# Performance work log

Hardware: AMD Instinct MI355X
Metric: run time of the kernel (lower is better)

The kernel has to match this reference:

```python
import jax, jax.numpy as jnp
import numpy as np

NUM_HEADS = 16
HEAD_DIM = 64  # embedding_dim 1024 / 16


def setup_inputs() -> dict:
    key = jax.random.key(0)
    k1, k2, k3, k4 = jax.random.split(key, 4)
    B, S, D = 2, 2048, 1024
    return {
        "query": jax.random.normal(k1, (B, S, D), dtype=jnp.float32),
        "key": jax.random.normal(k2, (B, S, D), dtype=jnp.float32),
        "value": jax.random.normal(k3, (B, S, D), dtype=jnp.float32),
        "W_out": jax.random.normal(k4, (D, D), dtype=jnp.float32) * (1.0 / np.sqrt(D)),
        "b_out": jnp.zeros((D,), dtype=jnp.float32),
    }


def reference(query, key, value, W_out, b_out):
    B, S, D = query.shape
    H, hd = NUM_HEADS, HEAD_DIM
    # NOTE: original forward never applies q_fc/k_fc/v_fc (transform ignores fc)
    q = query.reshape(B, S, H, hd).transpose(0, 2, 1, 3)  # [B,H,S,hd]
    k = key.reshape(B, S, H, hd).transpose(0, 2, 1, 3)
    v = value.reshape(B, S, H, hd).transpose(0, 2, 1, 3)
    scores = jnp.einsum("bhqd,bhkd->bhqk", q, k) / jnp.sqrt(jnp.float32(hd))
    probs = jax.nn.softmax(scores, axis=-1)  # mask=None, dropout=None
    ctx = jnp.einsum("bhqk,bhkd->bhqd", probs, v)
    ctx = ctx.transpose(0, 2, 1, 3).reshape(B, S, D)
    return ctx @ W_out.T + b_out
```

## Files before the change

### kernel.cpp

```cpp
#include <hip/hip_runtime.h>
#include <stdint.h>

#define NB 2
#define SEQ 2048
#define DIM 1024
#define NH 16
#define HD 64

typedef __attribute__((ext_vector_type(4))) float f32x4;
typedef __attribute__((ext_vector_type(16))) float f32x16;
typedef __attribute__((ext_vector_type(8))) short s16x8;
typedef __attribute__((ext_vector_type(4))) short s16x4;
typedef __attribute__((ext_vector_type(8))) __bf16 bf16x8;

static __device__ __forceinline__ short f2bf_rne(float x) {
  uint32_t u = __float_as_uint(x);
  u += 0x7fffu + ((u >> 16) & 1u);
  return (short)(u >> 16);
}
static __device__ __forceinline__ float bfbits2f(short h) {
  return __uint_as_float(((uint32_t)(uint16_t)h) << 16);
}
static __device__ __forceinline__ bf16x8 ldfrag(const short* p) {
  bf16x8 r;
  __builtin_memcpy(&r, p, 16);
  return r;
}
static __device__ __forceinline__ void glds16(const short* g, short* l) {
  __builtin_amdgcn_global_load_lds(
      (const __attribute__((address_space(1))) uint32_t*)g,
      (__attribute__((address_space(3))) uint32_t*)l, 16, 0, 0);
}

__global__ __launch_bounds__(256) void prep_kv(const float* __restrict__ K,
                                               const float* __restrict__ V,
                                               short* __restrict__ Kh,
                                               short* __restrict__ Vt) {
  __shared__ float vtile[64][65];
  const int tid = threadIdx.x;
  const int t0 = blockIdx.x * 64;
  const int bh = blockIdx.y;
  const int b = bh >> 4, h = bh & 15;

#pragma unroll
  for (int i = 0; i < 4; ++i) {
    int f = tid + 256 * i;
    int row = f >> 4;
    int col = (f & 15) * 4;
    const float* src = K + ((size_t)(b * SEQ + t0 + row)) * DIM + h * HD + col;
    f32x4 v = *(const f32x4*)src;
    s16x4 hi;
#pragma unroll
    for (int j = 0; j < 4; ++j) hi[j] = f2bf_rne(v[j]);
    *(s16x4*)(Kh + ((size_t)bh * SEQ + t0 + row) * HD + col) = hi;
  }
#pragma unroll
  for (int i = 0; i < 4; ++i) {
    int f = tid + 256 * i;
    int row = f >> 4;
    int col = (f & 15) * 4;
    const float* src = V + ((size_t)(b * SEQ + t0 + row)) * DIM + h * HD + col;
    f32x4 v = *(const f32x4*)src;
#pragma unroll
    for (int j = 0; j < 4; ++j) vtile[row][col + j] = v[j];
  }
  __syncthreads();
#pragma unroll
  for (int i = 0; i < 4; ++i) {
    int idx = tid + 256 * i;
    int d = idx >> 4;
    int kb = (idx & 15) * 4;
    s16x4 o4;
#pragma unroll
    for (int j = 0; j < 4; ++j) o4[j] = f2bf_rne(vtile[kb + j][d]);
    *(s16x4*)(Vt + ((size_t)bh * HD + d) * SEQ + t0 + kb) = o4;
  }
}

__global__ __launch_bounds__(256) void prep_w(const float* __restrict__ W,
                                              short* __restrict__ Wh) {
  size_t idx = ((size_t)blockIdx.x * 256 + threadIdx.x) * 8;
  f32x4 a = *(const f32x4*)(W + idx);
  f32x4 b = *(const f32x4*)(W + idx + 4);
  s16x8 o;
#pragma unroll
  for (int j = 0; j < 4; ++j) {
    o[j] = f2bf_rne(a[j]);
    o[4 + j] = f2bf_rne(b[j]);
  }
  *(s16x8*)(Wh + idx) = o;
}

#define PST 72
#define QSCALE (0.125f * 1.44269504088896340736f)

__global__ __launch_bounds__(256, 2) void attn(const float* __restrict__ Q,
                                               const short* __restrict__ Kh,
                                               const short* __restrict__ Vt,
                                               short* __restrict__ Ch) {
  __shared__ __align__(16) short ksh[2][64 * 64];
  __shared__ __align__(16) short vts[2][64 * 64];
  __shared__ __align__(16) short pts[4 * 32 * PST];

  const int tid = threadIdx.x;
  const int wv = tid >> 6, ln = tid & 63;
  const int l32 = ln & 31, hl = ln >> 5;
  const int bh = blockIdx.y, b = bh >> 4, hh = bh & 15;
  const int q0 = blockIdx.x * 128 + wv * 32;

  bf16x8 qh[4], ql[4];
  {
    const float* qp = Q + ((size_t)(b * SEQ + q0 + l32)) * DIM + hh * HD + hl * 8;
#pragma unroll
    for (int ks = 0; ks < 4; ++ks) {
      short th[8], tl[8];
#pragma unroll
      for (int j = 0; j < 8; ++j) {
        float x = qp[ks * 16 + j] * QSCALE;
        short hs = f2bf_rne(x);
        th[j] = hs;
        tl[j] = f2bf_rne(x - bfbits2f(hs));
      }
      __builtin_memcpy(&qh[ks], th, 16);
      __builtin_memcpy(&ql[ks], tl, 16);
    }
  }

  f32x16 acc[2];
  float den[16];
#pragma unroll
  for (int r = 0; r < 16; ++r) {
    acc[0][r] = 0.f;
    acc[1][r] = 0.f;
    den[r] = 0.f;
  }

  short* pm = pts + wv * 32 * PST;
  const short* khg = Kh + (size_t)bh * SEQ * HD;
  const short* vtg = Vt + (size_t)bh * HD * SEQ;

  const int srow8 = ln >> 3;
  const int sg = ln & 7;
  const int ssw = (sg ^ (srow8 & 7)) * 8;

#pragma unroll
  for (int i = 0; i < 4; ++i) {
    int c = wv * 4 + i;
    int row = (c & 7) * 8 + srow8;
    int sw = (sg ^ (row & 7)) * 8;
    if (c < 8)
      glds16(khg + (size_t)row * HD + sw, &ksh[0][(c & 7) * 512]);
    else
      glds16(vtg + (size_t)row * SEQ + sw, &vts[0][(c & 7) * 512]);
  }

  for (int t = 0; t < SEQ / 64; ++t) {
    __syncthreads();
    if (t + 1 < SEQ / 64) {
      const int kk = (t + 1) * 64;
      const int bn = (t + 1) & 1;
#pragma unroll
      for (int i = 0; i < 4; ++i) {
        int c = wv * 4 + i;
        int row = (c & 7) * 8 + srow8;
        int sw = (sg ^ (row & 7)) * 8;
        if (c < 8)
          glds16(khg + (size_t)(kk + row) * HD + sw, &ksh[bn][(c & 7) * 512]);
        else
          glds16(vtg + (size_t)row * SEQ + kk + sw, &vts[bn][(c & 7) * 512]);
      }
    }
    const short* kb = ksh[t & 1];
    const short* vbuf = vts[t & 1];

#pragma unroll
    for (int nt = 0; nt < 2; ++nt) {
      f32x16 sf;
#pragma unroll
      for (int r = 0; r < 16; ++r) sf[r] = 0.f;
#pragma unroll
      for (int ks = 0; ks < 4; ++ks) {
        bf16x8 kf =
            ldfrag(kb + (nt * 32 + l32) * 64 + (((ks * 2 + hl) ^ (l32 & 7)) * 8));
        sf = __builtin_amdgcn_mfma_f32_32x32x16_bf16(qh[ks], kf, sf, 0, 0, 0);
        sf = __builtin_amdgcn_mfma_f32_32x32x16_bf16(ql[ks], kf, sf, 0, 0, 0);
      }
#pragma unroll
      for (int r = 0; r < 16; ++r) {
        float p = __builtin_amdgcn_exp2f(sf[r]);
        den[r] += p;
        int row = (r & 3) + 8 * (r >> 2) + 4 * hl;
        uint32_t u = __float_as_uint(p) + 0x8000u;
        pm[row * PST + nt * 32 + l32] = (short)(u >> 16);
      }
    }

#pragma unroll
    for (int ks = 0; ks < 4; ++ks) {
      bf16x8 pa = ldfrag(pm + l32 * PST + ks * 16 + hl * 8);
#pragma unroll
      for (int dt = 0; dt < 2; ++dt) {
        bf16x8 vf = ldfrag(vbuf + (dt * 32 + l32) * 64 +
                           (((ks * 2 + hl) ^ (l32 & 7)) * 8));
        acc[dt] = __builtin_amdgcn_mfma_f32_32x32x16_bf16(pa, vf, acc[dt], 0, 0, 0);
      }
    }
  }

#pragma unroll
  for (int r = 0; r < 16; ++r) {
    float d = den[r];
    d += __shfl_xor(d, 1);
    d += __shfl_xor(d, 2);
    d += __shfl_xor(d, 4);
    d += __shfl_xor(d, 8);
    d += __shfl_xor(d, 16);
    den[r] = 1.0f / d;
  }
#pragma unroll
  for (int dt = 0; dt < 2; ++dt)
#pragma unroll
    for (int r = 0; r < 16; ++r) {
      int row = (r & 3) + 8 * (r >> 2) + 4 * hl;
      size_t off = ((size_t)(b * SEQ + q0 + row)) * DIM + hh * HD + dt * 32 + l32;
      Ch[off] = f2bf_rne(acc[dt][r] * den[r]);
    }
}

__global__ __launch_bounds__(256, 2) void proj(const short* __restrict__ Ah,
                                               const short* __restrict__ Wh,
                                               const float* __restrict__ bias,
                                               float* __restrict__ OUT) {
  __shared__ __align__(16) short ash[2][128 * 64];
  __shared__ __align__(16) short wsh[2][128 * 64];
  const int tid = threadIdx.x;
  const int wv = tid >> 6, ln = tid & 63;
  const int l32 = ln & 31, hl = ln >> 5;
  const int wm = wv & 1, wn = wv >> 1;
  const int m0 = blockIdx.x * 128, n0 = blockIdx.y * 128;

  f32x16 acc[2][2];
#pragma unroll
  for (int mt = 0; mt < 2; ++mt)
#pragma unroll
    for (int nt = 0; nt < 2; ++nt)
#pragma unroll
      for (int r = 0; r < 16; ++r) acc[mt][nt][r] = 0.f;

  const int srow8 = ln >> 3, sg = ln & 7;

#pragma unroll
  for (int i = 0; i < 8; ++i) {
    int c = wv * 8 + i;
    int row = (c & 15) * 8 + srow8;
    int sw = (sg ^ (row & 7)) * 8;
    if (c < 16)
      glds16(Ah + (size_t)(m0 + row) * DIM + sw, &ash[0][(c & 15) * 512]);
    else
      glds16(Wh + (size_t)(n0 + row) * DIM + sw, &wsh[0][(c & 15) * 512]);
  }

  for (int kt = 0; kt < DIM / 64; ++kt) {
    __syncthreads();
    if (kt + 1 < DIM / 64) {
      const int kk = (kt + 1) * 64;
      const int bn = (kt + 1) & 1;
#pragma unroll
      for (int i = 0; i < 8; ++i) {
        int c = wv * 8 + i;
        int row = (c & 15) * 8 + srow8;
        int sw = (sg ^ (row & 7)) * 8;
        if (c < 16)
          glds16(Ah + (size_t)(m0 + row) * DIM + kk + sw, &ash[bn][(c & 15) * 512]);
        else
          glds16(Wh + (size_t)(n0 + row) * DIM + kk + sw, &wsh[bn][(c & 15) * 512]);
      }
    }
    const short* ab = ash[kt & 1];
    const short* wb = wsh[kt & 1];
#pragma unroll
    for (int ks = 0; ks < 4; ++ks) {
      bf16x8 af[2], wf[2];
#pragma unroll
      for (int mt = 0; mt < 2; ++mt)
        af[mt] = ldfrag(ab + (wm * 64 + mt * 32 + l32) * 64 +
                        (((ks * 2 + hl) ^ (l32 & 7)) * 8));
#pragma unroll
      for (int nt = 0; nt < 2; ++nt)
        wf[nt] = ldfrag(wb + (wn * 64 + nt * 32 + l32) * 64 +
                        (((ks * 2 + hl) ^ (l32 & 7)) * 8));
#pragma unroll
      for (int mt = 0; mt < 2; ++mt)
#pragma unroll
        for (int nt = 0; nt < 2; ++nt)
          acc[mt][nt] =
              __builtin_amdgcn_mfma_f32_32x32x16_bf16(af[mt], wf[nt], acc[mt][nt], 0, 0, 0);
    }
  }

  float bs[2];
#pragma unroll
  for (int nt = 0; nt < 2; ++nt) bs[nt] = bias[n0 + wn * 64 + nt * 32 + l32];
#pragma unroll
  for (int mt = 0; mt < 2; ++mt)
#pragma unroll
    for (int nt = 0; nt < 2; ++nt)
#pragma unroll
      for (int r = 0; r < 16; ++r) {
        int row = m0 + wm * 64 + mt * 32 + (r & 3) + 8 * (r >> 2) + 4 * hl;
        int col = n0 + wn * 64 + nt * 32 + l32;
        OUT[(size_t)row * DIM + col] = acc[mt][nt][r] + bs[nt];
      }
}

extern "C" void kernel_launch(void* const* d_in, const int* in_sizes, int n_in,
                              void* d_out, int out_size, void* d_ws, size_t ws_size,
                              hipStream_t stream) {
  const float* Q = (const float*)d_in[0];
  const float* K = (const float*)d_in[1];
  const float* V = (const float*)d_in[2];
  const float* W = (const float*)d_in[3];
  const float* bias = (const float*)d_in[4];
  float* OUT = (float*)d_out;

  char* ws = (char*)d_ws;
  short* Kh = (short*)(ws + ((size_t)0 << 20));
  short* Vt = (short*)(ws + ((size_t)8 << 20));
  short* Ch = (short*)(ws + ((size_t)16 << 20));
  short* Wh = (short*)(ws + ((size_t)24 << 20));

  prep_kv<<<dim3(SEQ / 64, NB * NH), 256, 0, stream>>>(K, V, Kh, Vt);
  prep_w<<<dim3((DIM * DIM) / 2048), 256, 0, stream>>>(W, Wh);
  attn<<<dim3(SEQ / 128, NB * NH), 256, 0, stream>>>(Q, Kh, Vt, Ch);
  proj<<<dim3((NB * SEQ) / 128, DIM / 128), 256, 0, stream>>>(Ch, Wh, bias, OUT);
}
```

Measured before the change: 178.0 us.

## Keep P in registers via transposed QK^T MFMA and permuted V layout; retile projection

The attention kernel now computes S^T by swapping the MFMA operands, so each lane's exp'd scores already form a valid A-operand fragment for the PV MFMA. This removes the per-wave LDS round trip for P and the PST scratch buffer. To match, prep_kv permutes the key order within each 16-chunk of Vt, and the softmax denominator becomes one scalar per lane redistributed by shuffles. The projection GEMM tile shrinks from 128x128 to 128x64 with one 32-row strip per wave, doubling the grid and lowering LDS per block, at the cost of less operand reuse per block.

```diff
diff --git a/kernel.cpp b/kernel.cpp
--- a/kernel.cpp
+++ b/kernel.cpp
@@ -70,10 +70,11 @@
     int idx = tid + 256 * i;
     int d = idx >> 4;
     int kb = (idx & 15) * 4;
+    int kp = (kb & ~12) | ((kb & 4) << 1) | ((kb & 8) >> 1);
     s16x4 o4;
 #pragma unroll
     for (int j = 0; j < 4; ++j) o4[j] = f2bf_rne(vtile[kb + j][d]);
-    *(s16x4*)(Vt + ((size_t)bh * HD + d) * SEQ + t0 + kb) = o4;
+    *(s16x4*)(Vt + ((size_t)bh * HD + d) * SEQ + t0 + kp) = o4;
   }
 }
 
@@ -91,7 +92,6 @@
   *(s16x8*)(Wh + idx) = o;
 }
 
-#define PST 72
 #define QSCALE (0.125f * 1.44269504088896340736f)
 
 __global__ __launch_bounds__(256, 2) void attn(const float* __restrict__ Q,
@@ -100,7 +100,6 @@
                                                short* __restrict__ Ch) {
   __shared__ __align__(16) short ksh[2][64 * 64];
   __shared__ __align__(16) short vts[2][64 * 64];
-  __shared__ __align__(16) short pts[4 * 32 * PST];
 
   const int tid = threadIdx.x;
   const int wv = tid >> 6, ln = tid & 63;
@@ -127,27 +126,24 @@
   }
 
   f32x16 acc[2];
-  float den[16];
 #pragma unroll
   for (int r = 0; r < 16; ++r) {
     acc[0][r] = 0.f;
     acc[1][r] = 0.f;
-    den[r] = 0.f;
-  }
-
-  short* pm = pts + wv * 32 * PST;
+  }
+  float den = 0.f;
+
   const short* khg = Kh + (size_t)bh * SEQ * HD;
   const short* vtg = Vt + (size_t)bh * HD * SEQ;
 
   const int srow8 = ln >> 3;
   const int sg = ln & 7;
-  const int ssw = (sg ^ (srow8 & 7)) * 8;
 
 #pragma unroll
   for (int i = 0; i < 4; ++i) {
     int c = wv * 4 + i;
     int row = (c & 7) * 8 + srow8;
-    int sw = (sg ^ (row & 7)) * 8;
+    int sw = (sg ^ srow8) * 8;
     if (c < 8)
       glds16(khg + (size_t)row * HD + sw, &ksh[0][(c & 7) * 512]);
     else
@@ -163,7 +159,7 @@
       for (int i = 0; i < 4; ++i) {
         int c = wv * 4 + i;
         int row = (c & 7) * 8 + srow8;
-        int sw = (sg ^ (row & 7)) * 8;
+        int sw = (sg ^ srow8) * 8;
         if (c < 8)
           glds16(khg + (size_t)(kk + row) * HD + sw, &ksh[bn][(c & 7) * 512]);
         else
@@ -182,48 +178,46 @@
       for (int ks = 0; ks < 4; ++ks) {
         bf16x8 kf =
             ldfrag(kb + (nt * 32 + l32) * 64 + (((ks * 2 + hl) ^ (l32 & 7)) * 8));
-        sf = __builtin_amdgcn_mfma_f32_32x32x16_bf16(qh[ks], kf, sf, 0, 0, 0);
-        sf = __builtin_amdgcn_mfma_f32_32x32x16_bf16(ql[ks], kf, sf, 0, 0, 0);
-      }
-#pragma unroll
-      for (int r = 0; r < 16; ++r) {
-        float p = __builtin_amdgcn_exp2f(sf[r]);
-        den[r] += p;
-        int row = (r & 3) + 8 * (r >> 2) + 4 * hl;
-        uint32_t u = __float_as_uint(p) + 0x8000u;
-        pm[row * PST + nt * 32 + l32] = (short)(u >> 16);
-      }
-    }
-
-#pragma unroll
-    for (int ks = 0; ks < 4; ++ks) {
-      bf16x8 pa = ldfrag(pm + l32 * PST + ks * 16 + hl * 8);
-#pragma unroll
-      for (int dt = 0; dt < 2; ++dt) {
-        bf16x8 vf = ldfrag(vbuf + (dt * 32 + l32) * 64 +
-                           (((ks * 2 + hl) ^ (l32 & 7)) * 8));
-        acc[dt] = __builtin_amdgcn_mfma_f32_32x32x16_bf16(pa, vf, acc[dt], 0, 0, 0);
-      }
-    }
-  }
-
-#pragma unroll
-  for (int r = 0; r < 16; ++r) {
-    float d = den[r];
-    d += __shfl_xor(d, 1);
-    d += __shfl_xor(d, 2);
-    d += __shfl_xor(d, 4);
-    d += __shfl_xor(d, 8);
-    d += __shfl_xor(d, 16);
-    den[r] = 1.0f / d;
-  }
+        sf = __builtin_amdgcn_mfma_f32_32x32x16_bf16(kf, qh[ks], sf, 0, 0, 0);
+        sf = __builtin_amdgcn_mfma_f32_32x32x16_bf16(kf, ql[ks], sf, 0, 0, 0);
+      }
+#pragma unroll
+      for (int tp = 0; tp < 2; ++tp) {
+        short pp[8];
+#pragma unroll
+        for (int j = 0; j < 8; ++j) {
+          float p = __builtin_amdgcn_exp2f(sf[tp * 8 + j]);
+          den += p;
+          uint32_t u = __float_as_uint(p) + 0x8000u;
+          pp[j] = (short)(u >> 16);
+        }
+        bf16x8 pa;
+        __builtin_memcpy(&pa, pp, 16);
+        const int ksg = nt * 2 + tp;
+#pragma unroll
+        for (int dt = 0; dt < 2; ++dt) {
+          bf16x8 vf = ldfrag(vbuf + (dt * 32 + l32) * 64 +
+                             (((ksg * 2 + hl) ^ (l32 & 7)) * 8));
+          acc[dt] =
+              __builtin_amdgcn_mfma_f32_32x32x16_bf16(pa, vf, acc[dt], 0, 0, 0);
+        }
+      }
+    }
+  }
+
+  den += __shfl_xor(den, 32);
+  float invd = 1.0f / den;
+  float inv_r[16];
+#pragma unroll
+  for (int r = 0; r < 16; ++r)
+    inv_r[r] = __shfl(invd, (r & 3) + 8 * (r >> 2) + 4 * hl, 64);
 #pragma unroll
   for (int dt = 0; dt < 2; ++dt)
 #pragma unroll
     for (int r = 0; r < 16; ++r) {
       int row = (r & 3) + 8 * (r >> 2) + 4 * hl;
       size_t off = ((size_t)(b * SEQ + q0 + row)) * DIM + hh * HD + dt * 32 + l32;
-      Ch[off] = f2bf_rne(acc[dt][r] * den[r]);
+      Ch[off] = f2bf_rne(acc[dt][r] * inv_r[r]);
     }
 }
 
@@ -232,32 +226,32 @@
                                                const float* __restrict__ bias,
                                                float* __restrict__ OUT) {
   __shared__ __align__(16) short ash[2][128 * 64];
-  __shared__ __align__(16) short wsh[2][128 * 64];
+  __shared__ __align__(16) short wsh[2][64 * 64];
   const int tid = threadIdx.x;
   const int wv = tid >> 6, ln = tid & 63;
   const int l32 = ln & 31, hl = ln >> 5;
-  const int wm = wv & 1, wn = wv >> 1;
-  const int m0 = blockIdx.x * 128, n0 = blockIdx.y * 128;
-
-  f32x16 acc[2][2];
-#pragma unroll
-  for (int mt = 0; mt < 2; ++mt)
-#pragma unroll
-    for (int nt = 0; nt < 2; ++nt)
-#pragma unroll
-      for (int r = 0; r < 16; ++r) acc[mt][nt][r] = 0.f;
+  const int m0 = blockIdx.x * 128, n0 = blockIdx.y * 64;
+
+  f32x16 acc[2];
+#pragma unroll
+  for (int r = 0; r < 16; ++r) {
+    acc[0][r] = 0.f;
+    acc[1][r] = 0.f;
+  }
 
   const int srow8 = ln >> 3, sg = ln & 7;
 
 #pragma unroll
-  for (int i = 0; i < 8; ++i) {
-    int c = wv * 8 + i;
-    int row = (c & 15) * 8 + srow8;
-    int sw = (sg ^ (row & 7)) * 8;
-    if (c < 16)
-      glds16(Ah + (size_t)(m0 + row) * DIM + sw, &ash[0][(c & 15) * 512]);
-    else
-      glds16(Wh + (size_t)(n0 + row) * DIM + sw, &wsh[0][(c & 15) * 512]);
+  for (int i = 0; i < 6; ++i) {
+    int c = wv * 6 + i;
+    int sw = (sg ^ srow8) * 8;
+    if (c < 16) {
+      int row = c * 8 + srow8;
+      glds16(Ah + (size_t)(m0 + row) * DIM + sw, &ash[0][c * 512]);
+    } else {
+      int row = (c - 16) * 8 + srow8;
+      glds16(Wh + (size_t)(n0 + row) * DIM + sw, &wsh[0][(c - 16) * 512]);
+    }
   }
 
   for (int kt = 0; kt < DIM / 64; ++kt) {
@@ -266,51 +260,43 @@
       const int kk = (kt + 1) * 64;
       const int bn = (kt + 1) & 1;
 #pragma unroll
-      for (int i = 0; i < 8; ++i) {
-        int c = wv * 8 + i;
-        int row = (c & 15) * 8 + srow8;
-        int sw = (sg ^ (row & 7)) * 8;
-        if (c < 16)
-          glds16(Ah + (size_t)(m0 + row) * DIM + kk + sw, &ash[bn][(c & 15) * 512]);
-        else
-          glds16(Wh + (size_t)(n0 + row) * DIM + kk + sw, &wsh[bn][(c & 15) * 512]);
+      for (int i = 0; i < 6; ++i) {
+        int c = wv * 6 + i;
+        int sw = (sg ^ srow8) * 8;
+        if (c < 16) {
+          int row = c * 8 + srow8;
+          glds16(Ah + (size_t)(m0 + row) * DIM + kk + sw, &ash[bn][c * 512]);
+        } else {
+          int row = (c - 16) * 8 + srow8;
+          glds16(Wh + (size_t)(n0 + row) * DIM + kk + sw, &wsh[bn][(c - 16) * 512]);
+        }
       }
     }
     const short* ab = ash[kt & 1];
     const short* wb = wsh[kt & 1];
 #pragma unroll
     for (int ks = 0; ks < 4; ++ks) {
-      bf16x8 af[2], wf[2];
-#pragma unroll
-      for (int mt = 0; mt < 2; ++mt)
-        af[mt] = ldfrag(ab + (wm * 64 + mt * 32 + l32) * 64 +
-                        (((ks * 2 + hl) ^ (l32 & 7)) * 8));
-#pragma unroll
-      for (int nt = 0; nt < 2; ++nt)
-        wf[nt] = ldfrag(wb + (wn * 64 + nt * 32 + l32) * 64 +
-                        (((ks * 2 + hl) ^ (l32 & 7)) * 8));
-#pragma unroll
-      for (int mt = 0; mt < 2; ++mt)
-#pragma unroll
-        for (int nt = 0; nt < 2; ++nt)
-          acc[mt][nt] =
-              __builtin_amdgcn_mfma_f32_32x32x16_bf16(af[mt], wf[nt], acc[mt][nt], 0, 0, 0);
+      bf16x8 af = ldfrag(ab + (wv * 32 + l32) * 64 + (((ks * 2 + hl) ^ (l32 & 7)) * 8));
+#pragma unroll
+      for (int nt = 0; nt < 2; ++nt) {
+        bf16x8 wf =
+            ldfrag(wb + (nt * 32 + l32) * 64 + (((ks * 2 + hl) ^ (l32 & 7)) * 8));
+        acc[nt] = __builtin_amdgcn_mfma_f32_32x32x16_bf16(af, wf, acc[nt], 0, 0, 0);
+      }
     }
   }
 
   float bs[2];
 #pragma unroll
-  for (int nt = 0; nt < 2; ++nt) bs[nt] = bias[n0 + wn * 64 + nt * 32 + l32];
-#pragma unroll
-  for (int mt = 0; mt < 2; ++mt)
-#pragma unroll
-    for (int nt = 0; nt < 2; ++nt)
-#pragma unroll
-      for (int r = 0; r < 16; ++r) {
-        int row = m0 + wm * 64 + mt * 32 + (r & 3) + 8 * (r >> 2) + 4 * hl;
-        int col = n0 + wn * 64 + nt * 32 + l32;
-        OUT[(size_t)row * DIM + col] = acc[mt][nt][r] + bs[nt];
-      }
+  for (int nt = 0; nt < 2; ++nt) bs[nt] = bias[n0 + nt * 32 + l32];
+#pragma unroll
+  for (int nt = 0; nt < 2; ++nt)
+#pragma unroll
+    for (int r = 0; r < 16; ++r) {
+      int row = m0 + wv * 32 + (r & 3) + 8 * (r >> 2) + 4 * hl;
+      int col = n0 + nt * 32 + l32;
+      OUT[(size_t)row * DIM + col] = acc[nt][r] + bs[nt];
+    }
 }
 
 extern "C" void kernel_launch(void* const* d_in, const int* in_sizes, int n_in,
@@ -332,5 +318,5 @@
   prep_kv<<<dim3(SEQ / 64, NB * NH), 256, 0, stream>>>(K, V, Kh, Vt);
   prep_w<<<dim3((DIM * DIM) / 2048), 256, 0, stream>>>(W, Wh);
   attn<<<dim3(SEQ / 128, NB * NH), 256, 0, stream>>>(Q, Kh, Vt, Ch);
-  proj<<<dim3((NB * SEQ) / 128, DIM / 128), 256, 0, stream>>>(Ch, Wh, bias, OUT);
-}
+  proj<<<dim3((NB * SEQ) / 128, DIM / 64), 256, 0, stream>>>(Ch, Wh, bias, OUT);
+}
```

Measured after the change: 171.5 us. 1.04x faster.
